# Optimization experiments

Measured on AMD Instinct MI355X. Metric: run time of the kernel, lower is better.

Reference implementation:

```python
import jax, jax.numpy as jnp
import numpy as np

EPS = 1e-5
FH, FW, OC = 1, 9, 32  # filt_h, filt_w, out_channels (hardcoded in HypER)


def _bn(x, g, b, axes):
    # training-mode batchnorm: biased variance over `axes`
    m = jnp.mean(x, axis=axes, keepdims=True)
    v = jnp.mean(jnp.square(x - m), axis=axes, keepdims=True)
    return (x - m) * jax.lax.rsqrt(v + EPS) * g + b


def setup_inputs() -> dict:
    key = jax.random.key(0)
    ks = jax.random.split(key, 8)
    N, INPUT_D, D1, D2, B = 50000, 400, 400, 400, 8192
    fc_len = OC * (D1 - FW + 1)  # 32*392 = 12544
    return {
        "head_tail_id": jax.random.randint(ks[0], (2, B), 0, N, dtype=jnp.int32),
        "unique_entity_embed": jax.random.normal(ks[1], (N, INPUT_D), jnp.float32),
        "W_E": jax.random.normal(ks[2], (INPUT_D, D1), jnp.float32) * 0.05,
        "fc1_w": jax.random.normal(ks[3], (OC * FW, D2), jnp.float32) * 0.05,
        "fc1_b": jnp.zeros((OC * FW,), jnp.float32),
        "fc_w": jax.random.normal(ks[4], (D1, fc_len), jnp.float32) * 0.02,
        "fc_b": jnp.zeros((D1,), jnp.float32),
        "bn0_g": jnp.ones((1,), jnp.float32),
        "bn0_b": jnp.zeros((1,), jnp.float32),
        "bn1_g": jnp.ones((OC,), jnp.float32),
        "bn1_b": jnp.zeros((OC,), jnp.float32),
        "bn2_g": jnp.ones((400,), jnp.float32),
        "bn2_b": jnp.zeros((400,), jnp.float32),
    }


def reference(head_tail_id, unique_entity_embed, W_E, fc1_w, fc1_b, fc_w, fc_b,
              bn0_g, bn0_b, bn1_g, bn1_b, bn2_g, bn2_b):
    E = unique_entity_embed @ W_E                    # (N, d1)
    head = E[head_tail_id[0]]                        # (B, d1)
    tail = E[head_tail_id[1]]                        # (B, d1)
    # bn0: BatchNorm2d with 1 channel -> normalize over all B*1*d1 elements
    x = _bn(head, bn0_g[0], bn0_b[0], axes=(0, 1))   # (B, d1)
    # hypernetwork: per-sample dynamic 1x9 filters for 32 out-channels
    k = (tail @ fc1_w.T + fc1_b).reshape(-1, OC, FW)  # (B, 32, 9)
    W_out = x.shape[1] - FW + 1                       # d1-8 = 392
    win_idx = jnp.arange(W_out)[:, None] + jnp.arange(FW)[None, :]
    xw = x[:, win_idx]                                # (B, W_out, 9) sliding windows
    # grouped conv (groups=B), cross-correlation as in F.conv2d
    conv = jnp.einsum('bjw,bow->boj', xw, k)          # (B, 32, W_out)
    # bn1: per out-channel over (B, W_out)
    conv = _bn(conv, bn1_g[None, :, None], bn1_b[None, :, None], axes=(0, 2))
    feat = conv.reshape(conv.shape[0], -1)            # (B, 32*W_out), channel-major flatten
    out = feat @ fc_w.T + fc_b                        # (B, d1)
    out = _bn(out, bn2_g, bn2_b, axes=(0,))           # BatchNorm1d over batch
    return jax.nn.relu(out)
```

## Files before the change

kernel.cpp:

```cpp
#include <hip/hip_runtime.h>


#define BB   8192
#define DD   400
#define RR   288
#define OCC  32
#define FWW  9
#define JJ   392
#define FCLEN 12544
#define KSPL 4
#define KS   (FCLEN / KSPL)
#define KSTEPS (KS / 64)
#define EPSF 1e-5

typedef __attribute__((ext_vector_type(8))) short bf16x8;
typedef __attribute__((ext_vector_type(4))) float f32x4;

__device__ inline unsigned short f2bf(float f) {
    union { float f; unsigned u; } x; x.f = f;
    unsigned r = x.u + 0x7fffu + ((x.u >> 16) & 1u);
    return (unsigned short)(r >> 16);
}

__device__ inline void gload16(const void* g, void* l) {
    __builtin_amdgcn_global_load_lds((const __attribute__((address_space(1))) unsigned int*)g,
                                     (__attribute__((address_space(3))) unsigned int*)l, 16, 0, 0);
}

__device__ inline float block_reduce_256(float v, float* red) {
    #pragma unroll
    for (int m = 1; m < 64; m <<= 1) v += __shfl_xor(v, m);
    int wv = threadIdx.x >> 6;
    if ((threadIdx.x & 63) == 0) red[wv] = v;
    __syncthreads();
    float r = 0.f;
    if (threadIdx.x == 0) r = red[0] + red[1] + red[2] + red[3];
    return r;
}

__global__ __launch_bounds__(256) void prep_M(const float* __restrict__ WE,
                                              const float* __restrict__ f1w,
                                              float* __restrict__ Mout) {
    __shared__ float sA[16][17];
    __shared__ float sB[16][17];
    int tx = threadIdx.x, ty = threadIdx.y;
    int r0 = blockIdx.x * 16, i0 = blockIdx.y * 16;
    float acc = 0.f;
    for (int d0 = 0; d0 < DD; d0 += 16) {
        sA[ty][tx] = WE[(size_t)(i0 + ty) * DD + d0 + tx];
        sB[ty][tx] = f1w[(size_t)(r0 + ty) * DD + d0 + tx];
        __syncthreads();
        #pragma unroll
        for (int dd = 0; dd < 16; ++dd) acc = fmaf(sA[ty][dd], sB[tx][dd], acc);
        __syncthreads();
    }
    Mout[(size_t)(i0 + ty) * RR + r0 + tx] = acc;
}

template <int BN>
__global__ __launch_bounds__(256) void gemm_s1(const float* __restrict__ A,
                                               const int* __restrict__ idx,
                                               const float* __restrict__ Bm,
                                               const float* __restrict__ bias,
                                               float* __restrict__ C, int N,
                                               float* __restrict__ bn0part) {
    constexpr int BNF = BN / 16;
    constexpr int BCH = 64 * (BN / 4) / 256;
    __shared__ unsigned short Al[64][72];
    __shared__ unsigned short Bl[BN][72];
    __shared__ int ridx[64];
    __shared__ float red[8];
    int tid = threadIdx.x;
    int bm = blockIdx.x, bn = blockIdx.y;
    if (tid < 64) ridx[tid] = idx[bm * 64 + tid];
    int lane = tid & 63, wv = tid >> 6;
    int m16 = lane & 15, kb = lane >> 4;
    f32x4 acc[BNF];
    #pragma unroll
    for (int nb = 0; nb < BNF; ++nb) acc[nb] = (f32x4){0.f, 0.f, 0.f, 0.f};
    __syncthreads();

    float4 av[4];
    float4 bv[BCH];
    auto LOADR = [&](int k0) {
        #pragma unroll
        for (int r = 0; r < 4; ++r) {
            int c = tid + 256 * r;
            int row = c >> 4, kq = c & 15;
            int gk = k0 + kq * 4;
            av[r] = (float4){0.f, 0.f, 0.f, 0.f};
            if (gk < DD) av[r] = *(const float4*)(A + (size_t)ridx[row] * DD + gk);
        }
        #pragma unroll
        for (int r = 0; r < BCH; ++r) {
            int c = tid + 256 * r;
            int kk2 = c / (BN / 4), nq = c % (BN / 4);
            int gk = k0 + kk2;
            bv[r] = (float4){0.f, 0.f, 0.f, 0.f};
            if (gk < DD) bv[r] = *(const float4*)(Bm + (size_t)gk * N + bn * BN + nq * 4);
        }
    };
    auto WRITELDS = [&]() {
        #pragma unroll
        for (int r = 0; r < 4; ++r) {
            int c = tid + 256 * r;
            int row = c >> 4, kq = c & 15;
            ushort4 p;
            p.x = f2bf(av[r].x); p.y = f2bf(av[r].y); p.z = f2bf(av[r].z); p.w = f2bf(av[r].w);
            *(ushort4*)&Al[row][kq * 4] = p;
        }
        #pragma unroll
        for (int r = 0; r < BCH; ++r) {
            int c = tid + 256 * r;
            int kk2 = c / (BN / 4), nq = c % (BN / 4);
            Bl[nq * 4 + 0][kk2] = f2bf(bv[r].x);
            Bl[nq * 4 + 1][kk2] = f2bf(bv[r].y);
            Bl[nq * 4 + 2][kk2] = f2bf(bv[r].z);
            Bl[nq * 4 + 3][kk2] = f2bf(bv[r].w);
        }
    };

    LOADR(0);
    for (int kt = 0; kt < 7; ++kt) {
        WRITELDS();
        __syncthreads();
        if (kt + 1 < 7) LOADR((kt + 1) * 64);
        #pragma unroll
        for (int ks = 0; ks < 2; ++ks) {
            bf16x8 a = *(const bf16x8*)&Al[wv * 16 + m16][ks * 32 + kb * 8];
            #pragma unroll
            for (int nb = 0; nb < BNF; ++nb) {
                bf16x8 b = *(const bf16x8*)&Bl[nb * 16 + m16][ks * 32 + kb * 8];
                acc[nb] = __builtin_amdgcn_mfma_f32_16x16x32_bf16(a, b, acc[nb], 0, 0, 0);
            }
        }
        __syncthreads();
    }
    float s1 = 0.f, s2 = 0.f;
    #pragma unroll
    for (int nb = 0; nb < BNF; ++nb)
        #pragma unroll
        for (int rr = 0; rr < 4; ++rr) {
            int gr = bm * 64 + wv * 16 + kb * 4 + rr;
            int gc = bn * BN + nb * 16 + m16;
            float v = acc[nb][rr];
            if (bias) v += bias[gc];
            C[(size_t)gr * N + gc] = v;
            s1 += v; s2 = fmaf(v, v, s2);
        }
    if (bn0part) {
        float t1 = block_reduce_256(s1, red);
        __syncthreads();
        float t2 = block_reduce_256(s2, red);
        if (tid == 0) {
            int pid = bm * gridDim.y + bn;
            bn0part[pid * 2] = t1; bn0part[pid * 2 + 1] = t2;
        }
    }
}

__global__ __launch_bounds__(256) void bn0_fin(const float* __restrict__ part,
                                               const float* __restrict__ g,
                                               const float* __restrict__ b,
                                               float* __restrict__ ab0) {
    __shared__ float red[8];
    float s1 = 0.f, s2 = 0.f;
    for (int i = threadIdx.x; i < 640; i += 256) {
        s1 += part[i * 2]; s2 += part[i * 2 + 1];
    }
    float t1 = block_reduce_256(s1, red);
    __syncthreads();
    float t2 = block_reduce_256(s2, red);
    if (threadIdx.x == 0) {
        double n = (double)BB * DD;
        double mean = (double)t1 / n;
        double var = (double)t2 / n - mean * mean;
        float a0 = (float)((double)g[0] / sqrt(var + EPSF));
        float b0 = (float)((double)b[0] - mean * a0);
        ab0[0] = a0; ab0[1] = b0;
    }
}

__global__ __launch_bounds__(256) void conv_k(const float* __restrict__ head,
                                              const float* __restrict__ kbuf,
                                              const float* __restrict__ ab0,
                                              unsigned short* __restrict__ convb,
                                              float* __restrict__ chpartT) {
    __shared__ float xs[DD];
    __shared__ float ks[RR];
    int b = blockIdx.x, tid = threadIdx.x;
    float a0 = ab0[0], b0 = ab0[1];
    for (int i = tid; i < DD; i += 256) xs[i] = fmaf(head[(size_t)b * DD + i], a0, b0);
    for (int i = tid; i < RR; i += 256) ks[i] = kbuf[(size_t)b * RR + i];
    __syncthreads();
    int lane = tid & 63, wv = tid >> 6;
    unsigned short* orow = convb + (size_t)b * FCLEN;
    float kk[8][FWW];
    #pragma unroll
    for (int oi = 0; oi < 8; ++oi)
        #pragma unroll
        for (int w2 = 0; w2 < FWW; ++w2) kk[oi][w2] = ks[(wv * 8 + oi) * FWW + w2];
    float s1[8], s2[8];
    #pragma unroll
    for (int oi = 0; oi < 8; ++oi) { s1[oi] = 0.f; s2[oi] = 0.f; }
    #pragma unroll
    for (int jt = 0; jt < 2; ++jt) {
        int j0 = jt * 256 + lane * 4;
        if (j0 < JJ) {
            const float4* x4 = (const float4*)xs;
            float4 va = x4[(j0 >> 2)], vb = x4[(j0 >> 2) + 1], vc = x4[(j0 >> 2) + 2];
            float x[12] = {va.x, va.y, va.z, va.w, vb.x, vb.y, vb.z, vb.w, vc.x, vc.y, vc.z, vc.w};
            #pragma unroll
            for (int oi = 0; oi < 8; ++oi) {
                float acc[4];
                #pragma unroll
                for (int q = 0; q < 4; ++q) {
                    float a = 0.f;
                    #pragma unroll
                    for (int w2 = 0; w2 < FWW; ++w2) a = fmaf(x[q + w2], kk[oi][w2], a);
                    acc[q] = a;
                }
                ushort4 p;
                p.x = f2bf(acc[0]); p.y = f2bf(acc[1]); p.z = f2bf(acc[2]); p.w = f2bf(acc[3]);
                *(ushort4*)(orow + (wv * 8 + oi) * JJ + j0) = p;
                #pragma unroll
                for (int q = 0; q < 4; ++q) { s1[oi] += acc[q]; s2[oi] = fmaf(acc[q], acc[q], s2[oi]); }
            }
        }
    }
    #pragma unroll
    for (int oi = 0; oi < 8; ++oi) {
        float a = s1[oi], c = s2[oi];
        #pragma unroll
        for (int m = 1; m < 64; m <<= 1) { a += __shfl_xor(a, m); c += __shfl_xor(c, m); }
        if (lane == 0) {
            int o = wv * 8 + oi;
            chpartT[(size_t)o * BB + b] = a;
            chpartT[(size_t)(OCC + o) * BB + b] = c;
        }
    }
}

__global__ __launch_bounds__(256) void bn1_fin(const float* __restrict__ chpartT,
                                               const float* __restrict__ g1,
                                               const float* __restrict__ b1,
                                               float* __restrict__ alphabeta) {
    __shared__ float red[8];
    int o = blockIdx.x, tid = threadIdx.x;
    float s1 = 0.f, s2 = 0.f;
    for (int t = tid; t < BB; t += 256) {
        s1 += chpartT[(size_t)o * BB + t];
        s2 += chpartT[(size_t)(OCC + o) * BB + t];
    }
    float t1 = block_reduce_256(s1, red);
    __syncthreads();
    float t2 = block_reduce_256(s2, red);
    if (tid == 0) {
        double n = (double)BB * JJ;
        double mean = (double)t1 / n;
        double var = (double)t2 / n - mean * mean;
        float al = (float)((double)g1[o] / sqrt(var + EPSF));
        float be = (float)((double)b1[o] - mean * al);
        alphabeta[o] = al; alphabeta[OCC + o] = be;
    }
}

__global__ __launch_bounds__(256) void prep_fcw(const float* __restrict__ fc_w,
                                                const float* __restrict__ fc_b,
                                                const float* __restrict__ alphabeta,
                                                unsigned short* __restrict__ Bp,
                                                float* __restrict__ bias2) {
    __shared__ float al[OCC], be[OCC];
    __shared__ float red[8];
    int d = blockIdx.x, tid = threadIdx.x;
    if (tid < OCC) { al[tid] = alphabeta[tid]; be[tid] = alphabeta[OCC + tid]; }
    __syncthreads();
    const float* row = fc_w + (size_t)d * FCLEN;
    unsigned short* orow = Bp + (size_t)d * FCLEN;
    float bacc = 0.f;
    for (int o = 0; o < OCC; ++o) {
        float a = al[o], bb = be[o];
        for (int j = tid; j < JJ; j += 256) {
            float wv = row[o * JJ + j];
            orow[o * JJ + j] = f2bf(wv * a);
            bacc = fmaf(wv, bb, bacc);
        }
    }
    float t = block_reduce_256(bacc, red);
    if (tid == 0) bias2[d] = fc_b[d] + t;
}

__global__ __launch_bounds__(256, 3) void fc_gemm_sk(const unsigned short* __restrict__ A,
                                                     const unsigned short* __restrict__ Bp,
                                                     float* __restrict__ P) {
    __shared__ __align__(16) unsigned short Al[256 * 64];
    __shared__ __align__(16) unsigned short Bl[80 * 64];
    int tid = threadIdx.x;
    int bm = blockIdx.x, bn = blockIdx.y, bz = blockIdx.z;
    int lane = tid & 63, wv = tid >> 6;
    int m16 = lane & 15, kb = lane >> 4;
    int srow = lane >> 3, scol = lane & 7;
    int sw = m16 & 7;
    f32x4 acc[4][5];
    #pragma unroll
    for (int mi = 0; mi < 4; ++mi)
        #pragma unroll
        for (int nb = 0; nb < 5; ++nb) acc[mi][nb] = (f32x4){0.f, 0.f, 0.f, 0.f};

    const unsigned short* Asrc = A + (size_t)(bm * 256 + srow) * FCLEN
                                   + (size_t)bz * KS + ((scol ^ srow) << 3);
    const unsigned short* Bsrc = Bp + (size_t)(bn * 80 + srow) * FCLEN
                                   + (size_t)bz * KS + ((scol ^ srow) << 3);

    for (int kt = 0; kt < KSTEPS; ++kt) {
        const size_t koff = (size_t)kt * 64;
        #pragma unroll
        for (int i = 0; i < 11; ++i) {
            int c = wv + i * 4;
            if (c < 32) {
                gload16(Asrc + (size_t)c * 8 * FCLEN + koff, Al + c * 512);
            } else if (c < 42) {
                int cb = c - 32;
                gload16(Bsrc + (size_t)cb * 8 * FCLEN + koff, Bl + cb * 512);
            }
        }
        __syncthreads();
        #pragma unroll
        for (int ks2 = 0; ks2 < 2; ++ks2) {
            int ch = (((ks2 * 4 + kb) ^ sw) << 3);
            bf16x8 a[4];
            #pragma unroll
            for (int mi = 0; mi < 4; ++mi)
                a[mi] = *(const bf16x8*)(Al + (wv * 64 + mi * 16 + m16) * 64 + ch);
            #pragma unroll
            for (int nb = 0; nb < 5; ++nb) {
                bf16x8 b = *(const bf16x8*)(Bl + (nb * 16 + m16) * 64 + ch);
                #pragma unroll
                for (int mi = 0; mi < 4; ++mi)
                    acc[mi][nb] = __builtin_amdgcn_mfma_f32_16x16x32_bf16(a[mi], b, acc[mi][nb], 0, 0, 0);
            }
        }
        __syncthreads();
    }

    float* Po = P + (size_t)bz * BB * DD;
    #pragma unroll
    for (int mi = 0; mi < 4; ++mi)
        #pragma unroll
        for (int nb = 0; nb < 5; ++nb)
            #pragma unroll
            for (int rr = 0; rr < 4; ++rr) {
                int gr = bm * 256 + wv * 64 + mi * 16 + kb * 4 + rr;
                int gc = bn * 80 + nb * 16 + m16;
                Po[(size_t)gr * DD + gc] = acc[mi][nb][rr];
            }
}

__global__ __launch_bounds__(256) void reduce_bn2(const float* __restrict__ P,
                                                  const float* __restrict__ bias2,
                                                  float* __restrict__ out,
                                                  float* __restrict__ part) {
    int blk = blockIdx.x, tid = threadIdx.x;
    int r0 = blk * 64;
    const size_t S = (size_t)BB * DD;
    bool hasb = tid < DD - 256;
    float bia = bias2[tid];
    float bib = hasb ? bias2[256 + tid] : 0.f;
    float s1a = 0.f, s2a = 0.f, s1b = 0.f, s2b = 0.f;
    for (int r = 0; r < 64; ++r) {
        size_t base = (size_t)(r0 + r) * DD;
        float v = P[base + tid] + P[S + base + tid] + P[2 * S + base + tid] + P[3 * S + base + tid] + bia;
        out[base + tid] = v;
        s1a += v; s2a = fmaf(v, v, s2a);
        if (hasb) {
            size_t b2i = base + 256 + tid;
            float u = P[b2i] + P[S + b2i] + P[2 * S + b2i] + P[3 * S + b2i] + bib;
            out[b2i] = u;
            s1b += u; s2b = fmaf(u, u, s2b);
        }
    }
    float* p = part + (size_t)blk * (DD * 2);
    p[tid * 2] = s1a; p[tid * 2 + 1] = s2a;
    if (hasb) { p[(256 + tid) * 2] = s1b; p[(256 + tid) * 2 + 1] = s2b; }
}

__global__ __launch_bounds__(128) void bn2_fin(const float* __restrict__ part,
                                               const float* __restrict__ g2,
                                               const float* __restrict__ b2,
                                               float* __restrict__ sc,
                                               float* __restrict__ sh) {
    __shared__ float red[4];
    int col = blockIdx.x, tid = threadIdx.x;
    float s1 = part[(size_t)tid * (DD * 2) + col * 2];
    float s2 = part[(size_t)tid * (DD * 2) + col * 2 + 1];
    #pragma unroll
    for (int m = 1; m < 64; m <<= 1) { s1 += __shfl_xor(s1, m); s2 += __shfl_xor(s2, m); }
    int wv = tid >> 6;
    if ((tid & 63) == 0) { red[wv] = s1; red[2 + wv] = s2; }
    __syncthreads();
    if (tid == 0) {
        double t1 = (double)red[0] + red[1];
        double t2 = (double)red[2] + red[3];
        double mean = t1 / (double)BB;
        double var = t2 / (double)BB - mean * mean;
        float s = (float)((double)g2[col] / sqrt(var + EPSF));
        sc[col] = s;
        sh[col] = (float)((double)b2[col] - mean * s);
    }
}

__global__ __launch_bounds__(256) void final_k(float* __restrict__ out,
                                               const float* __restrict__ sc,
                                               const float* __restrict__ sh) {
    __shared__ float lsc[DD], lsh[DD];
    int tid = threadIdx.x;
    for (int c = tid; c < DD; c += 256) { lsc[c] = sc[c]; lsh[c] = sh[c]; }
    __syncthreads();
    size_t base = (size_t)blockIdx.x * 4 * DD;
    for (int r = 0; r < 4; ++r)
        for (int c = tid; c < DD; c += 256) {
            size_t i = base + (size_t)r * DD + c;
            float v = fmaf(out[i], lsc[c], lsh[c]);
            out[i] = v > 0.f ? v : 0.f;
        }
}

extern "C" void kernel_launch(void* const* d_in, const int* in_sizes, int n_in,
                              void* d_out, int out_size, void* d_ws, size_t ws_size,
                              hipStream_t stream) {
    const int* ht      = (const int*)d_in[0];
    const float* UE    = (const float*)d_in[1];
    const float* W_E   = (const float*)d_in[2];
    const float* fc1_w = (const float*)d_in[3];
    const float* fc1_b = (const float*)d_in[4];
    const float* fc_w  = (const float*)d_in[5];
    const float* fc_b  = (const float*)d_in[6];
    const float* bn0_g = (const float*)d_in[7];
    const float* bn0_b = (const float*)d_in[8];
    const float* bn1_g = (const float*)d_in[9];
    const float* bn1_b = (const float*)d_in[10];
    const float* bn2_g = (const float*)d_in[11];
    const float* bn2_b = (const float*)d_in[12];
    float* out = (float*)d_out;

    char* w = (char*)d_ws;
    unsigned short* convb = (unsigned short*)w; w += (size_t)BB * FCLEN * 2;
    unsigned short* Bprep = (unsigned short*)w; w += (size_t)DD * FCLEN * 2;
    float* chpartT = (float*)w; w += (size_t)2 * OCC * BB * 4;
    float* bn0p = (float*)w;  w += 640 * 2 * 4;
    float* ab0 = (float*)w;   w += 64;
    float* alphabeta = (float*)w; w += 64 * 4;
    float* bias2 = (float*)w; w += DD * 4;
    float* bn2p = (float*)w;  w += (size_t)128 * DD * 2 * 4;
    float* bn2sc = (float*)w; w += DD * 4;
    float* bn2sh = (float*)w; w += DD * 4;
    float* P = (float*)w;     w += (size_t)KSPL * BB * DD * 4;
    float* head = P;
    float* kbuf = head + (size_t)BB * DD;
    float* Mbuf = kbuf + (size_t)BB * RR;
    (void)ws_size; (void)in_sizes; (void)n_in; (void)out_size;

    prep_M<<<dim3(RR / 16, DD / 16), dim3(16, 16), 0, stream>>>(W_E, fc1_w, Mbuf);
    gemm_s1<80><<<dim3(BB / 64, DD / 80), 256, 0, stream>>>(UE, ht, W_E, nullptr, head, DD, bn0p);
    gemm_s1<96><<<dim3(BB / 64, RR / 96), 256, 0, stream>>>(UE, ht + BB, Mbuf, fc1_b, kbuf, RR, nullptr);
    bn0_fin<<<1, 256, 0, stream>>>(bn0p, bn0_g, bn0_b, ab0);
    conv_k<<<BB, 256, 0, stream>>>(head, kbuf, ab0, convb, chpartT);
    bn1_fin<<<OCC, 256, 0, stream>>>(chpartT, bn1_g, bn1_b, alphabeta);
    prep_fcw<<<DD, 256, 0, stream>>>(fc_w, fc_b, alphabeta, Bprep, bias2);
    fc_gemm_sk<<<dim3(BB / 256, DD / 80, KSPL), 256, 0, stream>>>(convb, Bprep, P);
    reduce_bn2<<<128, 256, 0, stream>>>(P, bias2, out, bn2p);
    bn2_fin<<<DD, 128, 0, stream>>>(bn2p, bn2_g, bn2_b, bn2sc, bn2sh);
    final_k<<<2048, 256, 0, stream>>>(out, bn2sc, bn2sh);
}
```

Baseline: 359.2 us.

## Double-buffer fc GEMM with smaller M tiles, XCD-aware block remap, wider bn2 reduction

The split-K fc GEMM now uses a 128-row M tile with double-buffered LDS, prefetching the next K step while MFMAs run on the current one. It also raises wave priority around the MFMA section and remaps a flat 1D grid so that blocks are spread across the XCDs. The bn2 reduction launches 512 blocks of 16 rows each instead of 128 blocks of 64, and the finalize kernel loops over the larger partial buffer. Together these aim to improve latency hiding and occupancy in the dominant GEMM and to parallelize the reduction. The cost is more redundant loading of the B tile and more partial sums to combine.

```diff
diff --git a/kernel.cpp b/kernel.cpp
--- a/kernel.cpp
+++ b/kernel.cpp
@@ -12,6 +12,7 @@
 #define KS   (FCLEN / KSPL)
 #define KSTEPS (KS / 64)
 #define EPSF 1e-5
+#define RB2  512
 
 typedef __attribute__((ext_vector_type(8))) short bf16x8;
 typedef __attribute__((ext_vector_type(4))) float f32x4;
@@ -293,64 +294,78 @@
 __global__ __launch_bounds__(256, 3) void fc_gemm_sk(const unsigned short* __restrict__ A,
                                                      const unsigned short* __restrict__ Bp,
                                                      float* __restrict__ P) {
-    __shared__ __align__(16) unsigned short Al[256 * 64];
-    __shared__ __align__(16) unsigned short Bl[80 * 64];
+    __shared__ __align__(16) unsigned short Al[2][128 * 64];
+    __shared__ __align__(16) unsigned short Bl[2][80 * 64];
     int tid = threadIdx.x;
-    int bm = blockIdx.x, bn = blockIdx.y, bz = blockIdx.z;
+    int orig = blockIdx.x;
+    int wgid = (orig & 7) * 160 + (orig >> 3);
+    int bn = wgid % 5;
+    int rest = wgid / 5;
+    int bm = rest & 63;
+    int bz = rest >> 6;
     int lane = tid & 63, wv = tid >> 6;
     int m16 = lane & 15, kb = lane >> 4;
     int srow = lane >> 3, scol = lane & 7;
     int sw = m16 & 7;
-    f32x4 acc[4][5];
-    #pragma unroll
-    for (int mi = 0; mi < 4; ++mi)
+    f32x4 acc[2][5];
+    #pragma unroll
+    for (int mi = 0; mi < 2; ++mi)
         #pragma unroll
         for (int nb = 0; nb < 5; ++nb) acc[mi][nb] = (f32x4){0.f, 0.f, 0.f, 0.f};
 
-    const unsigned short* Asrc = A + (size_t)(bm * 256 + srow) * FCLEN
+    const unsigned short* Asrc = A + (size_t)(bm * 128 + srow) * FCLEN
                                    + (size_t)bz * KS + ((scol ^ srow) << 3);
     const unsigned short* Bsrc = Bp + (size_t)(bn * 80 + srow) * FCLEN
                                    + (size_t)bz * KS + ((scol ^ srow) << 3);
 
-    for (int kt = 0; kt < KSTEPS; ++kt) {
-        const size_t koff = (size_t)kt * 64;
-        #pragma unroll
-        for (int i = 0; i < 11; ++i) {
+    auto STAGE = [&](int t, int buf) {
+        const size_t koff = (size_t)t * 64;
+        #pragma unroll
+        for (int i = 0; i < 7; ++i) {
             int c = wv + i * 4;
-            if (c < 32) {
-                gload16(Asrc + (size_t)c * 8 * FCLEN + koff, Al + c * 512);
-            } else if (c < 42) {
-                int cb = c - 32;
-                gload16(Bsrc + (size_t)cb * 8 * FCLEN + koff, Bl + cb * 512);
+            if (c < 16) {
+                gload16(Asrc + (size_t)c * 8 * FCLEN + koff, &Al[buf][c * 512]);
+            } else if (c < 26) {
+                int cb = c - 16;
+                gload16(Bsrc + (size_t)cb * 8 * FCLEN + koff, &Bl[buf][cb * 512]);
             }
         }
-        __syncthreads();
+    };
+
+    STAGE(0, 0);
+    __syncthreads();
+    for (int t = 0; t < KSTEPS; ++t) {
+        if (t + 1 < KSTEPS) STAGE(t + 1, (t + 1) & 1);
+        const unsigned short* Ac = &Al[t & 1][0];
+        const unsigned short* Bc = &Bl[t & 1][0];
+        __builtin_amdgcn_s_setprio(1);
         #pragma unroll
         for (int ks2 = 0; ks2 < 2; ++ks2) {
             int ch = (((ks2 * 4 + kb) ^ sw) << 3);
-            bf16x8 a[4];
+            bf16x8 a[2];
             #pragma unroll
-            for (int mi = 0; mi < 4; ++mi)
-                a[mi] = *(const bf16x8*)(Al + (wv * 64 + mi * 16 + m16) * 64 + ch);
+            for (int mi = 0; mi < 2; ++mi)
+                a[mi] = *(const bf16x8*)(Ac + (wv * 32 + mi * 16 + m16) * 64 + ch);
             #pragma unroll
             for (int nb = 0; nb < 5; ++nb) {
-                bf16x8 b = *(const bf16x8*)(Bl + (nb * 16 + m16) * 64 + ch);
+                bf16x8 b = *(const bf16x8*)(Bc + (nb * 16 + m16) * 64 + ch);
                 #pragma unroll
-                for (int mi = 0; mi < 4; ++mi)
+                for (int mi = 0; mi < 2; ++mi)
                     acc[mi][nb] = __builtin_amdgcn_mfma_f32_16x16x32_bf16(a[mi], b, acc[mi][nb], 0, 0, 0);
             }
         }
+        __builtin_amdgcn_s_setprio(0);
         __syncthreads();
     }
 
     float* Po = P + (size_t)bz * BB * DD;
     #pragma unroll
-    for (int mi = 0; mi < 4; ++mi)
+    for (int mi = 0; mi < 2; ++mi)
         #pragma unroll
         for (int nb = 0; nb < 5; ++nb)
             #pragma unroll
             for (int rr = 0; rr < 4; ++rr) {
-                int gr = bm * 256 + wv * 64 + mi * 16 + kb * 4 + rr;
+                int gr = bm * 128 + wv * 32 + mi * 16 + kb * 4 + rr;
                 int gc = bn * 80 + nb * 16 + m16;
                 Po[(size_t)gr * DD + gc] = acc[mi][nb][rr];
             }
@@ -361,13 +376,13 @@
                                                   float* __restrict__ out,
                                                   float* __restrict__ part) {
     int blk = blockIdx.x, tid = threadIdx.x;
-    int r0 = blk * 64;
+    int r0 = blk * 16;
     const size_t S = (size_t)BB * DD;
     bool hasb = tid < DD - 256;
     float bia = bias2[tid];
     float bib = hasb ? bias2[256 + tid] : 0.f;
     float s1a = 0.f, s2a = 0.f, s1b = 0.f, s2b = 0.f;
-    for (int r = 0; r < 64; ++r) {
+    for (int r = 0; r < 16; ++r) {
         size_t base = (size_t)(r0 + r) * DD;
         float v = P[base + tid] + P[S + base + tid] + P[2 * S + base + tid] + P[3 * S + base + tid] + bia;
         out[base + tid] = v;
@@ -391,8 +406,11 @@
                                                float* __restrict__ sh) {
     __shared__ float red[4];
     int col = blockIdx.x, tid = threadIdx.x;
-    float s1 = part[(size_t)tid * (DD * 2) + col * 2];
-    float s2 = part[(size_t)tid * (DD * 2) + col * 2 + 1];
+    float s1 = 0.f, s2 = 0.f;
+    for (int t = tid; t < RB2; t += 128) {
+        s1 += part[(size_t)t * (DD * 2) + col * 2];
+        s2 += part[(size_t)t * (DD * 2) + col * 2 + 1];
+    }
     #pragma unroll
     for (int m = 1; m < 64; m <<= 1) { s1 += __shfl_xor(s1, m); s2 += __shfl_xor(s2, m); }
     int wv = tid >> 6;
@@ -451,7 +469,7 @@
     float* ab0 = (float*)w;   w += 64;
     float* alphabeta = (float*)w; w += 64 * 4;
     float* bias2 = (float*)w; w += DD * 4;
-    float* bn2p = (float*)w;  w += (size_t)128 * DD * 2 * 4;
+    float* bn2p = (float*)w;  w += (size_t)RB2 * DD * 2 * 4;
     float* bn2sc = (float*)w; w += DD * 4;
     float* bn2sh = (float*)w; w += DD * 4;
     float* P = (float*)w;     w += (size_t)KSPL * BB * DD * 4;
@@ -467,8 +485,8 @@
     conv_k<<<BB, 256, 0, stream>>>(head, kbuf, ab0, convb, chpartT);
     bn1_fin<<<OCC, 256, 0, stream>>>(chpartT, bn1_g, bn1_b, alphabeta);
     prep_fcw<<<DD, 256, 0, stream>>>(fc_w, fc_b, alphabeta, Bprep, bias2);
-    fc_gemm_sk<<<dim3(BB / 256, DD / 80, KSPL), 256, 0, stream>>>(convb, Bprep, P);
-    reduce_bn2<<<128, 256, 0, stream>>>(P, bias2, out, bn2p);
+    fc_gemm_sk<<<dim3(64 * 5 * KSPL), 256, 0, stream>>>(convb, Bprep, P);
+    reduce_bn2<<<RB2, 256, 0, stream>>>(P, bias2, out, bn2p);
     bn2_fin<<<DD, 128, 0, stream>>>(bn2p, bn2_g, bn2_b, bn2sc, bn2sh);
     final_k<<<2048, 256, 0, stream>>>(out, bn2sc, bn2sh);
 }
```

New measurement: 350.1 us. -2.5%, faster.
